# Optimization experiments

Measured on AMD Instinct MI355X. Metric: run time of the kernel, lower is better.

## Reference

```python
import jax, jax.numpy as jnp
import numpy as np

ALPHA = 0.05


def setup_inputs() -> dict:
    key = jax.random.key(0)
    k1, k2, k3, k4 = jax.random.split(key, 4)
    B, C, D = 16384, 4096, 768
    logits = jax.random.normal(k1, (B, C), dtype=jnp.float32)
    targets = jax.random.randint(k2, (B,), 0, C, dtype=jnp.int64)
    prototypes = jax.random.normal(k3, (C, D), dtype=jnp.float32)
    boundaries = jax.random.uniform(k4, (C,), dtype=jnp.float32)
    return {"logits": logits, "targets": targets,
            "prototypes": prototypes, "boundaries": boundaries}


def _cross_entropy(logits, targets):
    # mean over batch of -log_softmax(logits)[target]
    logp = jax.nn.log_softmax(logits, axis=-1)
    nll = -jnp.take_along_axis(logp, targets[:, None], axis=-1)[:, 0]
    return jnp.mean(nll)


def _inter_class_constraint(prototypes, boundaries):
    C = prototypes.shape[0]
    # Gram matrix G[i, j] = p_i . p_j  replaces the O(C^2) python loop
    gram = prototypes @ prototypes.T                      # [C, C]
    diag = jnp.diagonal(gram)                             # p_i . p_i, [C]
    term1 = (1.0 - boundaries) * diag                     # [C], depends on i only
    term2 = (boundaries[None, :] - 1.0) * gram            # [C, C], b_j and G[i,j]
    constraint = term1[:, None] + term2                   # [C, C]
    off_diag = 1.0 - jnp.eye(C, dtype=constraint.dtype)
    ic_sum = jnp.sum(jax.nn.relu(constraint) * off_diag)
    count = C * (C - 1)
    return ic_sum / max(count, 1)


def reference(logits, targets, prototypes, boundaries):
    cls_loss = _cross_entropy(logits, targets)
    ic_loss = _inter_class_constraint(prototypes, boundaries)
    total_loss = cls_loss + ALPHA * ic_loss
    return (total_loss, cls_loss, ic_loss)
```

## Files before the change

kernel.cpp:

```cpp
#include <hip/hip_runtime.h>
#include <hip/hip_bf16.h>
#include <math.h>

#define NB 16384
#define NC 4096
#define ND 768
#define WS_NLL   0
#define WS_ICP   65536
#define WS_T1    69632
#define WS_P16   86016

typedef __bf16 bf16x8 __attribute__((ext_vector_type(8)));
typedef float  f32x4  __attribute__((ext_vector_type(4)));

__device__ __forceinline__ unsigned short f2bf(float f) {
    return __builtin_bit_cast(unsigned short, __float2bfloat16(f));
}

template<bool PRECONV>
__global__ __launch_bounds__(256) void prep_kernel(const float* __restrict__ prot,
                                                   const float* __restrict__ bnd,
                                                   float* __restrict__ t1,
                                                   unsigned short* __restrict__ P16) {
    int w = threadIdx.x >> 6;
    int lane = threadIdx.x & 63;
    int row = blockIdx.x * 4 + w;
    const float4* rp = reinterpret_cast<const float4*>(prot + (size_t)row * ND);
    float ss = 0.f;
#pragma unroll
    for (int it = 0; it < 3; ++it) {
        int idx = it * 64 + lane;
        float4 v = rp[idx];
        ss += v.x * v.x + v.y * v.y + v.z * v.z + v.w * v.w;
        if (PRECONV) {
            ushort4 h;
            h.x = f2bf(v.x); h.y = f2bf(v.y); h.z = f2bf(v.z); h.w = f2bf(v.w);
            *reinterpret_cast<ushort4*>(P16 + (size_t)row * ND + idx * 4) = h;
        }
    }
#pragma unroll
    for (int off = 32; off; off >>= 1) ss += __shfl_xor(ss, off);
    if (lane == 0) t1[row] = (1.f - bnd[row]) * ss;
}

__global__ __launch_bounds__(256) void ce_kernel(const float* __restrict__ logits,
                                                 const int* __restrict__ targets,
                                                 float* __restrict__ nll) {
    int row = blockIdx.x;
    int tid = threadIdx.x;
    const float4* rp = reinterpret_cast<const float4*>(logits + (size_t)row * NC);
    float4 v[4];
#pragma unroll
    for (int i = 0; i < 4; ++i) v[i] = rp[tid + 256 * i];
    float m = -3.4e38f;
#pragma unroll
    for (int i = 0; i < 4; ++i)
        m = fmaxf(m, fmaxf(fmaxf(v[i].x, v[i].y), fmaxf(v[i].z, v[i].w)));
    float s = 0.f;
#pragma unroll
    for (int i = 0; i < 4; ++i)
        s += __expf(v[i].x - m) + __expf(v[i].y - m) + __expf(v[i].z - m) + __expf(v[i].w - m);
#pragma unroll
    for (int off = 32; off; off >>= 1) {
        float mo = __shfl_xor(m, off);
        float so = __shfl_xor(s, off);
        float mn = fmaxf(m, mo);
        s = s * __expf(m - mn) + so * __expf(mo - mn);
        m = mn;
    }
    __shared__ float smx[4], ssm[4];
    int w = tid >> 6, lane = tid & 63;
    if (lane == 0) { smx[w] = m; ssm[w] = s; }
    __syncthreads();
    if (tid == 0) {
        float M = smx[0], S = ssm[0];
#pragma unroll
        for (int i = 1; i < 4; ++i) {
            float mn = fmaxf(M, smx[i]);
            S = S * __expf(M - mn) + ssm[i] * __expf(smx[i] - mn);
            M = mn;
        }
        int t = targets[row];
        float xt = logits[(size_t)row * NC + t];
        nll[row] = M + __logf(S) - xt;
    }
}

template<bool PRECONV>
__global__ __launch_bounds__(256) void ic_kernel(const unsigned short* __restrict__ P16,
                                                 const float* __restrict__ prot,
                                                 const float* __restrict__ bnd,
                                                 const float* __restrict__ t1,
                                                 float* __restrict__ ic_part) {
    __shared__ __bf16 As[128][72];
    __shared__ __bf16 Bs[128][72];
    int tid = threadIdx.x;
    int bi = blockIdx.x >> 5, bj = blockIdx.x & 31;
    int row0 = bi * 128, col0 = bj * 128;
    int lane = tid & 63, w = tid >> 6;
    int fr = lane & 15, fq = lane >> 4;
    int wrow = (w >> 1) * 64, wcol = (w & 1) * 64;

    f32x4 acc[4][4];
#pragma unroll
    for (int mi = 0; mi < 4; ++mi)
#pragma unroll
        for (int nj = 0; nj < 4; ++nj) acc[mi][nj] = (f32x4){0.f, 0.f, 0.f, 0.f};

    for (int kt = 0; kt < ND / 64; ++kt) {
        if (PRECONV) {
#pragma unroll
            for (int s2 = 0; s2 < 4; ++s2) {
                int c = tid + 256 * s2;
                int r = c >> 3, k8 = c & 7;
                uint4 va = *reinterpret_cast<const uint4*>(P16 + (size_t)(row0 + r) * ND + kt * 64 + k8 * 8);
                *reinterpret_cast<uint4*>(&As[r][k8 * 8]) = va;
                uint4 vb = *reinterpret_cast<const uint4*>(P16 + (size_t)(col0 + r) * ND + kt * 64 + k8 * 8);
                *reinterpret_cast<uint4*>(&Bs[r][k8 * 8]) = vb;
            }
        } else {
#pragma unroll
            for (int s2 = 0; s2 < 8; ++s2) {
                int c = tid + 256 * s2;
                int r = c >> 4, k4 = c & 15;
                float4 va = *reinterpret_cast<const float4*>(prot + (size_t)(row0 + r) * ND + kt * 64 + k4 * 4);
                ushort4 ha; ha.x = f2bf(va.x); ha.y = f2bf(va.y); ha.z = f2bf(va.z); ha.w = f2bf(va.w);
                *reinterpret_cast<ushort4*>(&As[r][k4 * 4]) = ha;
                float4 vb = *reinterpret_cast<const float4*>(prot + (size_t)(col0 + r) * ND + kt * 64 + k4 * 4);
                ushort4 hb; hb.x = f2bf(vb.x); hb.y = f2bf(vb.y); hb.z = f2bf(vb.z); hb.w = f2bf(vb.w);
                *reinterpret_cast<ushort4*>(&Bs[r][k4 * 4]) = hb;
            }
        }
        __syncthreads();
#pragma unroll
        for (int ks = 0; ks < 64; ks += 32) {
            bf16x8 af[4], bfv[4];
#pragma unroll
            for (int mi = 0; mi < 4; ++mi)
                af[mi] = *reinterpret_cast<const bf16x8*>(&As[wrow + mi * 16 + fr][ks + fq * 8]);
#pragma unroll
            for (int nj = 0; nj < 4; ++nj)
                bfv[nj] = *reinterpret_cast<const bf16x8*>(&Bs[wcol + nj * 16 + fr][ks + fq * 8]);
#pragma unroll
            for (int mi = 0; mi < 4; ++mi)
#pragma unroll
                for (int nj = 0; nj < 4; ++nj)
                    acc[mi][nj] = __builtin_amdgcn_mfma_f32_16x16x32_bf16(af[mi], bfv[nj], acc[mi][nj], 0, 0, 0);
        }
        __syncthreads();
    }

    float t1r[16];
#pragma unroll
    for (int mi = 0; mi < 4; ++mi)
#pragma unroll
        for (int e = 0; e < 4; ++e)
            t1r[mi * 4 + e] = t1[row0 + wrow + mi * 16 + fq * 4 + e];
    float cj[4];
#pragma unroll
    for (int nj = 0; nj < 4; ++nj) cj[nj] = bnd[col0 + wcol + nj * 16 + fr] - 1.f;

    float sum = 0.f;
#pragma unroll
    for (int mi = 0; mi < 4; ++mi) {
#pragma unroll
        for (int nj = 0; nj < 4; ++nj) {
#pragma unroll
            for (int e = 0; e < 4; ++e) {
                int i = row0 + wrow + mi * 16 + fq * 4 + e;
                int j = col0 + wcol + nj * 16 + fr;
                float con = t1r[mi * 4 + e] + cj[nj] * acc[mi][nj][e];
                if (i != j) sum += fmaxf(con, 0.f);
            }
        }
    }
#pragma unroll
    for (int off = 32; off; off >>= 1) sum += __shfl_xor(sum, off);
    __shared__ float bs[4];
    if (lane == 0) bs[w] = sum;
    __syncthreads();
    if (tid == 0) ic_part[blockIdx.x] = bs[0] + bs[1] + bs[2] + bs[3];
}

__global__ __launch_bounds__(1024) void fin_kernel(const float* __restrict__ nll,
                                                   const float* __restrict__ icp,
                                                   float* __restrict__ out) {
    int tid = threadIdx.x;
    double s = 0.0;
    for (int i = tid; i < NB; i += 1024) s += (double)nll[i];
    double s2 = (double)icp[tid];
#pragma unroll
    for (int off = 32; off; off >>= 1) {
        s  += __shfl_xor(s, off);
        s2 += __shfl_xor(s2, off);
    }
    __shared__ double sm[16], sm2[16];
    int w = tid >> 6, lane = tid & 63;
    if (lane == 0) { sm[w] = s; sm2[w] = s2; }
    __syncthreads();
    if (tid == 0) {
        double a = 0.0, b = 0.0;
        for (int i = 0; i < 16; ++i) { a += sm[i]; b += sm2[i]; }
        double cls = a / (double)NB;
        double ic  = b / ((double)NC * (double)(NC - 1));
        out[0] = (float)(cls + 0.05 * ic);
        out[1] = (float)cls;
        out[2] = (float)ic;
    }
}

extern "C" void kernel_launch(void* const* d_in, const int* in_sizes, int n_in,
                              void* d_out, int out_size, void* d_ws, size_t ws_size,
                              hipStream_t stream) {
    const float* logits  = (const float*)d_in[0];
    const int*   targets = (const int*)d_in[1];
    const float* prot    = (const float*)d_in[2];
    const float* bnd     = (const float*)d_in[3];
    float* out = (float*)d_out;
    char* ws = (char*)d_ws;
    float* nll = (float*)(ws + WS_NLL);
    float* icp = (float*)(ws + WS_ICP);
    float* t1  = (float*)(ws + WS_T1);
    unsigned short* P16 = (unsigned short*)(ws + WS_P16);
    bool pre = ws_size >= (size_t)WS_P16 + 2ull * NC * ND;

    ce_kernel<<<NB, 256, 0, stream>>>(logits, targets, nll);
    if (pre) {
        prep_kernel<true><<<NC / 4, 256, 0, stream>>>(prot, bnd, t1, P16);
        ic_kernel<true><<<1024, 256, 0, stream>>>(P16, prot, bnd, t1, icp);
    } else {
        prep_kernel<false><<<NC / 4, 256, 0, stream>>>(prot, bnd, t1, nullptr);
        ic_kernel<false><<<1024, 256, 0, stream>>>(nullptr, prot, bnd, t1, icp);
    }
    fin_kernel<<<1, 1024, 0, stream>>>(nll, icp, out);
}
```

Measured before the change: 88.74 us.

## Exploit Gram symmetry to compute only upper-triangular tiles in IC kernel

The IC kernel now launches one block per upper-triangular 128x128 tile pair instead of all tiles. Off-diagonal tiles evaluate both constraint(i,j) and constraint(j,i) from the same Gram value, which roughly halves the matrix-multiply and load work. The finalization kernel sums only the reduced set of partials, and the CE kernel launch is moved after the IC kernels. The tile index decode uses a small serial loop, and with fewer blocks the GPU may be less fully occupied.

```diff
diff --git a/kernel.cpp b/kernel.cpp
--- a/kernel.cpp
+++ b/kernel.cpp
@@ -1,14 +1,17 @@
 #include <hip/hip_runtime.h>
 #include <hip/hip_bf16.h>
-#include <math.h>
 
 #define NB 16384
 #define NC 4096
 #define ND 768
-#define WS_NLL   0
-#define WS_ICP   65536
-#define WS_T1    69632
-#define WS_P16   86016
+#define NT 32
+#define NIC 528
+
+#define WS_NLL 0
+#define WS_ICP 65536
+#define WS_T1  69632
+#define WS_P16 86016
+
 
 typedef __bf16 bf16x8 __attribute__((ext_vector_type(8)));
 typedef float  f32x4  __attribute__((ext_vector_type(4)));
@@ -91,15 +94,21 @@
                                                  const float* __restrict__ prot,
                                                  const float* __restrict__ bnd,
                                                  const float* __restrict__ t1,
-                                                 float* __restrict__ ic_part) {
+                                                 float* __restrict__ icp) {
     __shared__ __bf16 As[128][72];
     __shared__ __bf16 Bs[128][72];
-    int tid = threadIdx.x;
-    int bi = blockIdx.x >> 5, bj = blockIdx.x & 31;
-    int row0 = bi * 128, col0 = bj * 128;
-    int lane = tid & 63, w = tid >> 6;
-    int fr = lane & 15, fq = lane >> 4;
-    int wrow = (w >> 1) * 64, wcol = (w & 1) * 64;
+    const int tid = threadIdx.x;
+
+    const int icid = blockIdx.x;
+    int u = icid, bi = 0;
+    while (u >= NT - bi) { u -= NT - bi; ++bi; }
+    const int bj = bi + u;
+    const bool diag = (bi == bj);
+    const int row0 = bi * 128, col0 = bj * 128;
+
+    const int lane = tid & 63, w = tid >> 6;
+    const int fr = lane & 15, fq = lane >> 4;
+    const int wrow = (w >> 1) * 64, wcol = (w & 1) * 64;
 
     f32x4 acc[4][4];
 #pragma unroll
@@ -150,15 +159,22 @@
         __syncthreads();
     }
 
-    float t1r[16];
+    float t1a[16], ba1[16];
 #pragma unroll
     for (int mi = 0; mi < 4; ++mi)
 #pragma unroll
-        for (int e = 0; e < 4; ++e)
-            t1r[mi * 4 + e] = t1[row0 + wrow + mi * 16 + fq * 4 + e];
-    float cj[4];
-#pragma unroll
-    for (int nj = 0; nj < 4; ++nj) cj[nj] = bnd[col0 + wcol + nj * 16 + fr] - 1.f;
+        for (int e = 0; e < 4; ++e) {
+            int i = row0 + wrow + mi * 16 + fq * 4 + e;
+            t1a[mi * 4 + e] = t1[i];
+            ba1[mi * 4 + e] = bnd[i] - 1.f;
+        }
+    float t1b[4], bb1[4];
+#pragma unroll
+    for (int nj = 0; nj < 4; ++nj) {
+        int j = col0 + wcol + nj * 16 + fr;
+        t1b[nj] = t1[j];
+        bb1[nj] = bnd[j] - 1.f;
+    }
 
     float sum = 0.f;
 #pragma unroll
@@ -167,19 +183,25 @@
         for (int nj = 0; nj < 4; ++nj) {
 #pragma unroll
             for (int e = 0; e < 4; ++e) {
-                int i = row0 + wrow + mi * 16 + fq * 4 + e;
-                int j = col0 + wcol + nj * 16 + fr;
-                float con = t1r[mi * 4 + e] + cj[nj] * acc[mi][nj][e];
-                if (i != j) sum += fmaxf(con, 0.f);
+                float G = acc[mi][nj][e];
+                float tij = t1a[mi * 4 + e] + bb1[nj] * G;
+                if (diag) {
+                    int il = wrow + mi * 16 + fq * 4 + e;
+                    int jl = wcol + nj * 16 + fr;
+                    if (il != jl) sum += fmaxf(tij, 0.f);
+                } else {
+                    float tji = t1b[nj] + ba1[mi * 4 + e] * G;
+                    sum += fmaxf(tij, 0.f) + fmaxf(tji, 0.f);
+                }
             }
         }
     }
 #pragma unroll
     for (int off = 32; off; off >>= 1) sum += __shfl_xor(sum, off);
-    __shared__ float bs[4];
-    if (lane == 0) bs[w] = sum;
+    __shared__ float redf[4];
+    if (lane == 0) redf[w] = sum;
     __syncthreads();
-    if (tid == 0) ic_part[blockIdx.x] = bs[0] + bs[1] + bs[2] + bs[3];
+    if (tid == 0) icp[icid] = redf[0] + redf[1] + redf[2] + redf[3];
 }
 
 __global__ __launch_bounds__(1024) void fin_kernel(const float* __restrict__ nll,
@@ -188,7 +210,7 @@
     int tid = threadIdx.x;
     double s = 0.0;
     for (int i = tid; i < NB; i += 1024) s += (double)nll[i];
-    double s2 = (double)icp[tid];
+    double s2 = (tid < NIC) ? (double)icp[tid] : 0.0;
 #pragma unroll
     for (int off = 32; off; off >>= 1) {
         s  += __shfl_xor(s, off);
@@ -199,10 +221,10 @@
     if (lane == 0) { sm[w] = s; sm2[w] = s2; }
     __syncthreads();
     if (tid == 0) {
-        double a = 0.0, b = 0.0;
-        for (int i = 0; i < 16; ++i) { a += sm[i]; b += sm2[i]; }
+        double a = 0.0, c = 0.0;
+        for (int i = 0; i < 16; ++i) { a += sm[i]; c += sm2[i]; }
         double cls = a / (double)NB;
-        double ic  = b / ((double)NC * (double)(NC - 1));
+        double ic  = c / ((double)NC * (double)(NC - 1));
         out[0] = (float)(cls + 0.05 * ic);
         out[1] = (float)cls;
         out[2] = (float)ic;
@@ -224,13 +246,13 @@
     unsigned short* P16 = (unsigned short*)(ws + WS_P16);
     bool pre = ws_size >= (size_t)WS_P16 + 2ull * NC * ND;
 
-    ce_kernel<<<NB, 256, 0, stream>>>(logits, targets, nll);
     if (pre) {
         prep_kernel<true><<<NC / 4, 256, 0, stream>>>(prot, bnd, t1, P16);
-        ic_kernel<true><<<1024, 256, 0, stream>>>(P16, prot, bnd, t1, icp);
+        ic_kernel<true><<<NIC, 256, 0, stream>>>(P16, prot, bnd, t1, icp);
     } else {
         prep_kernel<false><<<NC / 4, 256, 0, stream>>>(prot, bnd, t1, nullptr);
-        ic_kernel<false><<<1024, 256, 0, stream>>>(nullptr, prot, bnd, t1, icp);
-    }
+        ic_kernel<false><<<NIC, 256, 0, stream>>>(nullptr, prot, bnd, t1, icp);
+    }
+    ce_kernel<<<NB, 256, 0, stream>>>(logits, targets, nll);
     fin_kernel<<<1, 1024, 0, stream>>>(nll, icp, out);
 }
```

Measured after the change: 91.28 us. 2.9% more time.
